# Optimization experiments

Hardware: AMD Instinct MI355X
Metric: run time of the kernel (lower is better)

Reference implementation:

```python
import jax, jax.numpy as jnp
import numpy as np

M, K, N = 2048, 4096, 11008
Q_ABS_MAX = 128.0  # x_scaled_abs_max_fp for w8a8
Q_MIN, Q_MAX = -128, 127


def setup_inputs() -> dict:
    key = jax.random.key(0)
    k1, k2, k3, k4 = jax.random.split(key, 4)
    x = jax.random.normal(k1, (M, K), dtype=jnp.float32)
    # pre-quantized int8 weight, stored [K, N] (transposed layout as in quantize_weights)
    w_q = jax.random.randint(k2, (K, N), Q_MIN, Q_MAX + 1, dtype=jnp.int32).astype(jnp.int8)
    bias = jax.random.normal(k3, (N,), dtype=jnp.float32) * 0.01
    # per-tensor weight dequant scale (q_scale of the quantized weight)
    y_scale = jax.random.uniform(k4, (1,), dtype=jnp.float32, minval=0.001, maxval=0.02)
    return {"x": x, "w_q": w_q, "bias": bias, "y_scale": y_scale}


def reference(x, w_q, bias, y_scale):
    # dynamic per-tensor activation quantization: scale = max|x| / 128
    x_scale = jnp.max(jnp.abs(x)) / jnp.float32(Q_ABS_MAX)
    x_q = jnp.clip(jnp.round(x / x_scale), Q_MIN, Q_MAX).astype(jnp.int8)
    c = jnp.matmul(x_q.astype(jnp.int32), w_q.astype(jnp.int32))
    # dequantize + bias
    y = c.astype(jnp.float32) * (x_scale * y_scale[0]) + bias
    return y
```

## Files before the change

### kernel.cpp

```cpp
#include <hip/hip_runtime.h>
#include <stdint.h>

#define M_DIM 2048
#define K_DIM 4096
#define N_DIM 11008

typedef int v4i __attribute__((ext_vector_type(4)));

#define WS_XQ_OFF   65536ull
#define WS_WT_OFF   8454144ull
#define WS_FULL_BYTES (8454144ull + 45088768ull)
#define WS_SMALL_BYTES 8454144ull

static __device__ __forceinline__ void llds16(const void* g, void* l) {
  __builtin_amdgcn_global_load_lds(
      reinterpret_cast<const uint32_t __attribute__((address_space(1)))*>(
          reinterpret_cast<uintptr_t>(g)),
      reinterpret_cast<uint32_t __attribute__((address_space(3)))*>(
          reinterpret_cast<uintptr_t>(l)),
      16, 0, 0);
}

__global__ __launch_bounds__(256) void absmax_kernel(const float* __restrict__ x,
                                                     float* __restrict__ part) {
  __shared__ float red[256];
  const int g = blockIdx.x * 256 + threadIdx.x;
  const float4* x4 = reinterpret_cast<const float4*>(x);
  float m = 0.f;
#pragma unroll
  for (int i = 0; i < 8; ++i) {
    float4 v = x4[(size_t)i * 262144 + g];
    m = fmaxf(m, fmaxf(fmaxf(fabsf(v.x), fabsf(v.y)),
                       fmaxf(fabsf(v.z), fabsf(v.w))));
  }
  red[threadIdx.x] = m;
  __syncthreads();
  for (int s = 128; s > 0; s >>= 1) {
    if (threadIdx.x < s) red[threadIdx.x] = fmaxf(red[threadIdx.x], red[threadIdx.x + s]);
    __syncthreads();
  }
  if (threadIdx.x == 0) part[blockIdx.x] = red[0];
}

__global__ __launch_bounds__(256) void finalize_scale(const float* __restrict__ part,
                                                      const float* __restrict__ y_scale,
                                                      float* __restrict__ scales) {
  __shared__ float red[256];
  const int t = threadIdx.x;
  float m = fmaxf(fmaxf(part[t], part[t + 256]), fmaxf(part[t + 512], part[t + 768]));
  red[t] = m;
  __syncthreads();
  for (int s = 128; s > 0; s >>= 1) {
    if (t < s) red[t] = fmaxf(red[t], red[t + s]);
    __syncthreads();
  }
  if (t == 0) {
    float xs = red[0] * (1.0f / 128.0f);
    scales[0] = xs;
    scales[1] = xs * y_scale[0];
  }
}

__global__ __launch_bounds__(256) void quant_kernel(const float* __restrict__ x,
                                                    const float* __restrict__ scales,
                                                    signed char* __restrict__ xq) {
  const float s = scales[0];
  const size_t t = (size_t)blockIdx.x * 256 + threadIdx.x;
  const float4* x4 = reinterpret_cast<const float4*>(x) + t * 4;
  v4i o;
#pragma unroll
  for (int i = 0; i < 4; ++i) {
    float4 v = x4[i];
    int q0 = (int)rintf(v.x / s);
    int q1 = (int)rintf(v.y / s);
    int q2 = (int)rintf(v.z / s);
    int q3 = (int)rintf(v.w / s);
    q0 = max(-128, min(127, q0));
    q1 = max(-128, min(127, q1));
    q2 = max(-128, min(127, q2));
    q3 = max(-128, min(127, q3));
    o[i] = (q0 & 255) | ((q1 & 255) << 8) | ((q2 & 255) << 16) | ((q3 & 255) << 24);
  }
  *reinterpret_cast<v4i*>(xq + t * 16) = o;
}

__global__ __launch_bounds__(256) void transpose_pack(const int* __restrict__ w,
                                                      signed char* __restrict__ wt) {
  __shared__ int tile[64 * 65];
  const int t = threadIdx.x;
  const int n0 = blockIdx.x * 64;
  const int k0 = blockIdx.y * 64;
#pragma unroll
  for (int p = 0; p < 4; ++p) {
    const int id = p * 256 + t;
    const int r = id >> 4;
    const int c4 = id & 15;
    v4i v = *reinterpret_cast<const v4i*>(w + (size_t)(k0 + r) * N_DIM + n0 + c4 * 4);
    tile[r * 65 + c4 * 4 + 0] = v[0];
    tile[r * 65 + c4 * 4 + 1] = v[1];
    tile[r * 65 + c4 * 4 + 2] = v[2];
    tile[r * 65 + c4 * 4 + 3] = v[3];
  }
  __syncthreads();
  const int nl = t >> 2;
  const int kseg = t & 3;
  v4i o;
#pragma unroll
  for (int q = 0; q < 4; ++q) {
    const int kb = kseg * 16 + q * 4;
    int b0 = tile[(kb + 0) * 65 + nl] & 255;
    int b1 = tile[(kb + 1) * 65 + nl] & 255;
    int b2 = tile[(kb + 2) * 65 + nl] & 255;
    int b3 = tile[(kb + 3) * 65 + nl] & 255;
    o[q] = b0 | (b1 << 8) | (b2 << 16) | (b3 << 24);
  }
  *reinterpret_cast<v4i*>(wt + (size_t)(n0 + nl) * K_DIM + k0 + kseg * 16) = o;
}

#define V4_TILE_B 24576
#define V4_NT     (K_DIM / 64)

__global__ __launch_bounds__(512, 4) void gemm_i8_v4(
    const signed char* __restrict__ xq, const signed char* __restrict__ wt,
    const float* __restrict__ scales, const float* __restrict__ bias,
    float* __restrict__ y) {
  __shared__ __align__(16) signed char smem[3 * V4_TILE_B];
  const int tid = threadIdx.x;

  const int bid = blockIdx.x;
  const int swz = (bid & 7) * 86 + (bid >> 3);
  const int m0 = (swz & 15) * 128;
  const int n0 = (swz >> 4) * 256;

  const int srow = tid >> 2;
  const int sseg = tid & 3;
  const int sgoff = (sseg ^ ((srow >> 1) & 3)) * 16;
  const signed char* gA  = xq + (size_t)(m0 + srow) * K_DIM + sgoff;
  const signed char* gB0 = wt + (size_t)(n0 + srow) * K_DIM + sgoff;
  const signed char* gB1 = wt + (size_t)(n0 + 128 + srow) * K_DIM + sgoff;
  signed char* const ldA  = smem + tid * 16;
  signed char* const ldB0 = smem + 8192 + tid * 16;
  signed char* const ldB1 = smem + 16384 + tid * 16;

#define STAGE(kt, soff)                                   \
  do {                                                    \
    const size_t ko_ = (size_t)(kt) * 64;                 \
    llds16(gA + ko_,  ldA + (soff));                      \
    llds16(gB0 + ko_, ldB0 + (soff));                     \
    llds16(gB1 + ko_, ldB1 + (soff));                     \
  } while (0)

  const int lane = tid & 63;
  const int wid = tid >> 6;
  const int wm = wid >> 2;
  const int wn = wid & 3;
  const int l15 = lane & 15;
  const int kc = lane >> 4;
  const int segoff = (kc ^ ((l15 >> 1) & 3)) * 16;
  const int offA = (wm * 64 + l15) * 64 + segoff;
  const int offB = 8192 + (wn * 64 + l15) * 64 + segoff;

  v4i acc[4][4] = {};

#define COMPUTE(roff)                                                        \
  do {                                                                       \
    const signed char* bp_ = smem + (roff);                                  \
    v4i a_[4], b_[4];                                                        \
    _Pragma("unroll")                                                        \
    for (int m_ = 0; m_ < 4; ++m_)                                           \
      a_[m_] = *reinterpret_cast<const v4i*>(bp_ + offA + m_ * 1024);        \
    _Pragma("unroll")                                                        \
    for (int n_ = 0; n_ < 4; ++n_)                                           \
      b_[n_] = *reinterpret_cast<const v4i*>(bp_ + offB + n_ * 1024);        \
    _Pragma("unroll")                                                        \
    for (int m_ = 0; m_ < 4; ++m_)                                           \
      _Pragma("unroll")                                                      \
      for (int n_ = 0; n_ < 4; ++n_)                                         \
        acc[m_][n_] = __builtin_amdgcn_mfma_i32_16x16x64_i8(                 \
            a_[m_], b_[n_], acc[m_][n_], 0, 0, 0);                           \
  } while (0)

  STAGE(0, 0);
  STAGE(1, V4_TILE_B);
  asm volatile("s_waitcnt vmcnt(3)" ::: "memory");
  __builtin_amdgcn_s_barrier();

  int rOff = 0;
  int sOff = 2 * V4_TILE_B;
  for (int t = 0; t < V4_NT - 2; ++t) {
    STAGE(t + 2, sOff);
    COMPUTE(rOff);
    asm volatile("s_waitcnt vmcnt(3)" ::: "memory");
    __builtin_amdgcn_s_barrier();
    rOff = (rOff == 2 * V4_TILE_B) ? 0 : rOff + V4_TILE_B;
    sOff = (sOff == 2 * V4_TILE_B) ? 0 : sOff + V4_TILE_B;
  }
  COMPUTE(rOff);
  asm volatile("s_waitcnt vmcnt(0)" ::: "memory");
  __builtin_amdgcn_s_barrier();
  rOff = (rOff == 2 * V4_TILE_B) ? 0 : rOff + V4_TILE_B;
  COMPUTE(rOff);

#undef STAGE
#undef COMPUTE

  const float s = scales[1];
#pragma unroll
  for (int n = 0; n < 4; ++n) {
    const int col = n0 + wn * 64 + n * 16 + l15;
    const float bv = bias[col];
#pragma unroll
    for (int m = 0; m < 4; ++m) {
      const int r0 = m0 + wm * 64 + m * 16 + kc * 4;
#pragma unroll
      for (int j = 0; j < 4; ++j)
        y[(size_t)(r0 + j) * N_DIM + col] = (float)acc[m][n][j] * s + bv;
    }
  }
}

#if defined(__has_builtin)
#if __has_builtin(__builtin_amdgcn_sdot4)
#define HAVE_SDOT4 1
#endif
#endif

static __device__ __forceinline__ int dot4(int a, int b, int c) {
#ifdef HAVE_SDOT4
  return __builtin_amdgcn_sdot4(a, b, c, false);
#else
  c += (int)(signed char)(a) * (int)(signed char)(b);
  c += (int)(signed char)(a >> 8) * (int)(signed char)(b >> 8);
  c += (int)(signed char)(a >> 16) * (int)(signed char)(b >> 16);
  c += (int)(signed char)(a >> 24) * (int)(signed char)(b >> 24);
  return c;
#endif
}

__global__ __launch_bounds__(256) void gemm_fallback(
    const signed char* __restrict__ xq, const int* __restrict__ w,
    const float* __restrict__ scales, const float* __restrict__ bias,
    float* __restrict__ y) {
  __shared__ int lds_a[64 * 17];
  __shared__ int lds_b[64 * 17];
  const int t = threadIdx.x;
  const int m0 = blockIdx.y * 64;
  const int n0 = blockIdx.x * 64;
  const int my = (t >> 4) * 4;
  const int nx = (t & 15) * 4;
  int acc[4][4] = {};
  for (int kt = 0; kt < K_DIM / 64; ++kt) {
    const int k0 = kt * 64;
    {
      const int r = t >> 2, sg = t & 3;
      v4i v = *reinterpret_cast<const v4i*>(xq + (size_t)(m0 + r) * K_DIM + k0 + sg * 16);
      lds_a[r * 17 + sg * 4 + 0] = v[0];
      lds_a[r * 17 + sg * 4 + 1] = v[1];
      lds_a[r * 17 + sg * 4 + 2] = v[2];
      lds_a[r * 17 + sg * 4 + 3] = v[3];
    }
    {
      const int n = t & 63, bkk = (t >> 6) * 4;
#pragma unroll
      for (int q = 0; q < 4; ++q) {
        const int kk = bkk + q;
        int b0 = w[(size_t)(k0 + kk * 4 + 0) * N_DIM + n0 + n] & 255;
        int b1 = w[(size_t)(k0 + kk * 4 + 1) * N_DIM + n0 + n] & 255;
        int b2 = w[(size_t)(k0 + kk * 4 + 2) * N_DIM + n0 + n] & 255;
        int b3 = w[(size_t)(k0 + kk * 4 + 3) * N_DIM + n0 + n] & 255;
        lds_b[n * 17 + kk] = b0 | (b1 << 8) | (b2 << 16) | (b3 << 24);
      }
    }
    __syncthreads();
#pragma unroll
    for (int kk = 0; kk < 16; ++kk) {
      int a[4], b[4];
#pragma unroll
      for (int i = 0; i < 4; ++i) a[i] = lds_a[(my + i) * 17 + kk];
#pragma unroll
      for (int j = 0; j < 4; ++j) b[j] = lds_b[(nx + j) * 17 + kk];
#pragma unroll
      for (int i = 0; i < 4; ++i)
#pragma unroll
        for (int j = 0; j < 4; ++j) acc[i][j] = dot4(a[i], b[j], acc[i][j]);
    }
    __syncthreads();
  }
  const float s = scales[1];
#pragma unroll
  for (int i = 0; i < 4; ++i)
#pragma unroll
    for (int j = 0; j < 4; ++j)
      y[(size_t)(m0 + my + i) * N_DIM + n0 + nx + j] =
          (float)acc[i][j] * s + bias[n0 + nx + j];
}

extern "C" void kernel_launch(void* const* d_in, const int* in_sizes, int n_in,
                              void* d_out, int out_size, void* d_ws, size_t ws_size,
                              hipStream_t stream) {
  (void)in_sizes; (void)n_in; (void)out_size;
  const float* x = (const float*)d_in[0];
  const int* w = (const int*)d_in[1];
  const float* bias = (const float*)d_in[2];
  const float* yscale = (const float*)d_in[3];
  float* y = (float*)d_out;
  char* ws = (char*)d_ws;
  float* scales = (float*)(ws);
  float* part = (float*)(ws + 1024);
  signed char* xq = (signed char*)(ws + WS_XQ_OFF);
  signed char* wt = (signed char*)(ws + WS_WT_OFF);

  if (ws_size < WS_SMALL_BYTES) return;

  absmax_kernel<<<1024, 256, 0, stream>>>(x, part);
  finalize_scale<<<1, 256, 0, stream>>>(part, yscale, scales);
  quant_kernel<<<2048, 256, 0, stream>>>(x, scales, xq);
  if (ws_size >= WS_FULL_BYTES) {
    transpose_pack<<<dim3(N_DIM / 64, K_DIM / 64), 256, 0, stream>>>(w, wt);
    gemm_i8_v4<<<(M_DIM / 128) * (N_DIM / 256), 512, 0, stream>>>(xq, wt, scales, bias, y);
  } else {
    gemm_fallback<<<dim3(N_DIM / 64, M_DIM / 64), 256, 0, stream>>>(xq, w, scales, bias, y);
  }
}
```

Before: 169.3 us.

## Shrink GEMM tile to 128x128 with 4 waves, unroll ring buffer, add setprio

The int8 GEMM block tile drops from 128x256 with 8 waves to 128x128 with 4 waves, doubling the grid, and the block swizzle is adjusted to match. The triple-buffer loop is fully unrolled by three so LDS offsets are constants rather than runtime selects. s_setprio is raised around the MFMA burst so math waves are favoured over loading waves. Smaller tiles give more blocks and better wave occupancy, but they reduce reuse of the A tile and increase global traffic per flop.

```diff
diff --git a/kernel.cpp b/kernel.cpp
--- a/kernel.cpp
+++ b/kernel.cpp
@@ -117,48 +117,47 @@
   *reinterpret_cast<v4i*>(wt + (size_t)(n0 + nl) * K_DIM + k0 + kseg * 16) = o;
 }
 
-#define V4_TILE_B 24576
-#define V4_NT     (K_DIM / 64)
-
-__global__ __launch_bounds__(512, 4) void gemm_i8_v4(
+#define V5_TILE_B 16384
+#define V5_NT     (K_DIM / 64)
+
+__global__ __launch_bounds__(256, 4) void gemm_i8_v5(
     const signed char* __restrict__ xq, const signed char* __restrict__ wt,
     const float* __restrict__ scales, const float* __restrict__ bias,
     float* __restrict__ y) {
-  __shared__ __align__(16) signed char smem[3 * V4_TILE_B];
+  __shared__ __align__(16) signed char smem[3 * V5_TILE_B];
   const int tid = threadIdx.x;
 
   const int bid = blockIdx.x;
-  const int swz = (bid & 7) * 86 + (bid >> 3);
+  const int swz = (bid & 7) * 172 + (bid >> 3);
   const int m0 = (swz & 15) * 128;
-  const int n0 = (swz >> 4) * 256;
+  const int n0 = (swz >> 4) * 128;
 
   const int srow = tid >> 2;
   const int sseg = tid & 3;
   const int sgoff = (sseg ^ ((srow >> 1) & 3)) * 16;
-  const signed char* gA  = xq + (size_t)(m0 + srow) * K_DIM + sgoff;
-  const signed char* gB0 = wt + (size_t)(n0 + srow) * K_DIM + sgoff;
-  const signed char* gB1 = wt + (size_t)(n0 + 128 + srow) * K_DIM + sgoff;
-  signed char* const ldA  = smem + tid * 16;
-  signed char* const ldB0 = smem + 8192 + tid * 16;
-  signed char* const ldB1 = smem + 16384 + tid * 16;
-
-#define STAGE(kt, soff)                                   \
-  do {                                                    \
-    const size_t ko_ = (size_t)(kt) * 64;                 \
-    llds16(gA + ko_,  ldA + (soff));                      \
-    llds16(gB0 + ko_, ldB0 + (soff));                     \
-    llds16(gB1 + ko_, ldB1 + (soff));                     \
+  const signed char* gA = xq + (size_t)(m0 + srow) * K_DIM + sgoff;
+  const signed char* gB = wt + (size_t)(n0 + srow) * K_DIM + sgoff;
+  signed char* const ldA = smem + tid * 16;
+  signed char* const ldB = smem + 8192 + tid * 16;
+
+#define STAGE(kt, soff)                                     \
+  do {                                                      \
+    const size_t ko_ = (size_t)(kt) * 64;                   \
+    llds16(gA + ko_,                      ldA + (soff));    \
+    llds16(gA + ko_ + (size_t)64 * K_DIM, ldA + (soff) + 4096); \
+    llds16(gB + ko_,                      ldB + (soff));    \
+    llds16(gB + ko_ + (size_t)64 * K_DIM, ldB + (soff) + 4096); \
   } while (0)
 
   const int lane = tid & 63;
   const int wid = tid >> 6;
-  const int wm = wid >> 2;
-  const int wn = wid & 3;
+  const int wr = wid >> 1;
+  const int wc = wid & 1;
   const int l15 = lane & 15;
   const int kc = lane >> 4;
   const int segoff = (kc ^ ((l15 >> 1) & 3)) * 16;
-  const int offA = (wm * 64 + l15) * 64 + segoff;
-  const int offB = 8192 + (wn * 64 + l15) * 64 + segoff;
+  const int offA = (wr * 64 + l15) * 64 + segoff;
+  const int offB = 8192 + (wc * 64 + l15) * 64 + segoff;
 
   v4i acc[4][4] = {};
 
@@ -172,46 +171,53 @@
     _Pragma("unroll")                                                        \
     for (int n_ = 0; n_ < 4; ++n_)                                           \
       b_[n_] = *reinterpret_cast<const v4i*>(bp_ + offB + n_ * 1024);        \
+    __builtin_amdgcn_s_setprio(1);                                           \
     _Pragma("unroll")                                                        \
     for (int m_ = 0; m_ < 4; ++m_)                                           \
       _Pragma("unroll")                                                      \
       for (int n_ = 0; n_ < 4; ++n_)                                         \
         acc[m_][n_] = __builtin_amdgcn_mfma_i32_16x16x64_i8(                 \
             a_[m_], b_[n_], acc[m_][n_], 0, 0, 0);                           \
+    __builtin_amdgcn_s_setprio(0);                                           \
   } while (0)
 
+#define ITER(R, S, kt2)                                     \
+  do {                                                      \
+    STAGE((kt2), (S));                                      \
+    COMPUTE((R));                                           \
+    asm volatile("s_waitcnt vmcnt(4)" ::: "memory");        \
+    __builtin_amdgcn_s_barrier();                           \
+  } while (0)
+
   STAGE(0, 0);
-  STAGE(1, V4_TILE_B);
-  asm volatile("s_waitcnt vmcnt(3)" ::: "memory");
+  STAGE(1, V5_TILE_B);
+  asm volatile("s_waitcnt vmcnt(4)" ::: "memory");
   __builtin_amdgcn_s_barrier();
 
-  int rOff = 0;
-  int sOff = 2 * V4_TILE_B;
-  for (int t = 0; t < V4_NT - 2; ++t) {
-    STAGE(t + 2, sOff);
-    COMPUTE(rOff);
-    asm volatile("s_waitcnt vmcnt(3)" ::: "memory");
-    __builtin_amdgcn_s_barrier();
-    rOff = (rOff == 2 * V4_TILE_B) ? 0 : rOff + V4_TILE_B;
-    sOff = (sOff == 2 * V4_TILE_B) ? 0 : sOff + V4_TILE_B;
-  }
-  COMPUTE(rOff);
+  for (int t = 0; t < 60; t += 3) {
+    ITER(0,              2 * V5_TILE_B, t + 2);
+    ITER(V5_TILE_B,      0,             t + 3);
+    ITER(2 * V5_TILE_B,  V5_TILE_B,     t + 4);
+  }
+  ITER(0,         2 * V5_TILE_B, 62);
+  ITER(V5_TILE_B, 0,             63);
+  COMPUTE(2 * V5_TILE_B);
   asm volatile("s_waitcnt vmcnt(0)" ::: "memory");
   __builtin_amdgcn_s_barrier();
-  rOff = (rOff == 2 * V4_TILE_B) ? 0 : rOff + V4_TILE_B;
-  COMPUTE(rOff);
+  COMPUTE(0);
 
 #undef STAGE
 #undef COMPUTE
+#undef ITER
 
   const float s = scales[1];
 #pragma unroll
   for (int n = 0; n < 4; ++n) {
-    const int col = n0 + wn * 64 + n * 16 + l15;
+    const int col = n0 + wc * 64 + n * 16 + l15;
     const float bv = bias[col];
 #pragma unroll
     for (int m = 0; m < 4; ++m) {
-      const int r0 = m0 + wm * 64 + m * 16 + kc * 4;
+      const int r0 = m0 + wr * 64 + m * 16 + kc * 4;
 #pragma unroll
       for (int j = 0; j < 4; ++j)
         y[(size_t)(r0 + j) * N_DIM + col] = (float)acc[m][n][j] * s + bv;
@@ -317,7 +323,7 @@
   quant_kernel<<<2048, 256, 0, stream>>>(x, scales, xq);
   if (ws_size >= WS_FULL_BYTES) {
     transpose_pack<<<dim3(N_DIM / 64, K_DIM / 64), 256, 0, stream>>>(w, wt);
-    gemm_i8_v4<<<(M_DIM / 128) * (N_DIM / 256), 512, 0, stream>>>(xq, wt, scales, bias, y);
+    gemm_i8_v5<<<(M_DIM / 128) * (N_DIM / 128), 256, 0, stream>>>(xq, wt, scales, bias, y);
   } else {
     gemm_fallback<<<dim3(N_DIM / 64, M_DIM / 64), 256, 0, stream>>>(xq, w, scales, bias, y);
   }
```

Measured after the change: 186.6 us. 10.2% more time.

## Pre-pack operands into MFMA fragment order and switch to 32x32x32 int8 MFMA

Applied to the files above, without the earlier changes.

The quantize and weight-transpose kernels now write A and B directly in the per-tile, per-lane fragment order the GEMM consumes. Each stage load becomes one contiguous 16-byte-per-thread copy, and the XOR swizzle is no longer needed. The GEMM switches from 16x16x64 MFMAs with a 4x4 accumulator grid to 32x32x32 MFMAs with a 2x2 grid, which cuts LDS reads per MFMA. In exchange the packing kernels have more complex index math, and the epilogue stores follow the 32x32 output layout.

```diff
diff --git a/kernel.cpp b/kernel.cpp
--- a/kernel.cpp
+++ b/kernel.cpp
@@ -5,7 +5,8 @@
 #define K_DIM 4096
 #define N_DIM 11008
 
-typedef int v4i __attribute__((ext_vector_type(4)));
+typedef int v4i  __attribute__((ext_vector_type(4)));
+typedef int v16i __attribute__((ext_vector_type(16)));
 
 #define WS_XQ_OFF   65536ull
 #define WS_WT_OFF   8454144ull
@@ -61,26 +62,44 @@
   }
 }
 
-__global__ __launch_bounds__(256) void quant_kernel(const float* __restrict__ x,
-                                                    const float* __restrict__ scales,
-                                                    signed char* __restrict__ xq) {
+static __device__ __forceinline__ int quant4(float4 v, float s) {
+  int q0 = (int)rintf(v.x / s);
+  int q1 = (int)rintf(v.y / s);
+  int q2 = (int)rintf(v.z / s);
+  int q3 = (int)rintf(v.w / s);
+  q0 = max(-128, min(127, q0));
+  q1 = max(-128, min(127, q1));
+  q2 = max(-128, min(127, q2));
+  q3 = max(-128, min(127, q3));
+  return (q0 & 255) | ((q1 & 255) << 8) | ((q2 & 255) << 16) | ((q3 & 255) << 24);
+}
+
+__global__ __launch_bounds__(256) void quant_pack(const float* __restrict__ x,
+                                                  const float* __restrict__ scales,
+                                                  signed char* __restrict__ xq) {
+  const float s = scales[0];
+  const int g = blockIdx.x * 256 + threadIdx.x;
+  const int mblk = g >> 15;
+  const int kt = (g >> 9) & 63;
+  const int u = g & 511;
+  const int row = mblk * 128 + ((u >> 7) & 3) * 32 + (u & 31);
+  const int kf = kt * 64 + ((u >> 6) & 1) * 32 + ((u >> 5) & 1) * 16;
+  const float4* xp = reinterpret_cast<const float4*>(x + (size_t)row * K_DIM + kf);
+  v4i o;
+#pragma unroll
+  for (int i = 0; i < 4; ++i) o[i] = quant4(xp[i], s);
+  *reinterpret_cast<v4i*>(xq + (size_t)g * 16) = o;
+}
+
+__global__ __launch_bounds__(256) void quant_rowmajor(const float* __restrict__ x,
+                                                      const float* __restrict__ scales,
+                                                      signed char* __restrict__ xq) {
   const float s = scales[0];
   const size_t t = (size_t)blockIdx.x * 256 + threadIdx.x;
   const float4* x4 = reinterpret_cast<const float4*>(x) + t * 4;
   v4i o;
 #pragma unroll
-  for (int i = 0; i < 4; ++i) {
-    float4 v = x4[i];
-    int q0 = (int)rintf(v.x / s);
-    int q1 = (int)rintf(v.y / s);
-    int q2 = (int)rintf(v.z / s);
-    int q3 = (int)rintf(v.w / s);
-    q0 = max(-128, min(127, q0));
-    q1 = max(-128, min(127, q1));
-    q2 = max(-128, min(127, q2));
-    q3 = max(-128, min(127, q3));
-    o[i] = (q0 & 255) | ((q1 & 255) << 8) | ((q2 & 255) << 16) | ((q3 & 255) << 24);
-  }
+  for (int i = 0; i < 4; ++i) o[i] = quant4(x4[i], s);
   *reinterpret_cast<v4i*>(xq + t * 16) = o;
 }
 
@@ -88,8 +107,10 @@
                                                       signed char* __restrict__ wt) {
   __shared__ int tile[64 * 65];
   const int t = threadIdx.x;
-  const int n0 = blockIdx.x * 64;
-  const int k0 = blockIdx.y * 64;
+  const int bx = blockIdx.x;
+  const int by = blockIdx.y;
+  const int n0 = bx * 64;
+  const int k0 = by * 64;
 #pragma unroll
   for (int p = 0; p < 4; ++p) {
     const int id = p * 256 + t;
@@ -102,119 +123,115 @@
     tile[r * 65 + c4 * 4 + 3] = v[3];
   }
   __syncthreads();
-  const int nl = t >> 2;
-  const int kseg = t & 3;
+  const int nl = ((t >> 7) << 5) | (t & 31);
+  const int kc = (t >> 5) & 3;
   v4i o;
 #pragma unroll
   for (int q = 0; q < 4; ++q) {
-    const int kb = kseg * 16 + q * 4;
+    const int kb = kc * 16 + q * 4;
     int b0 = tile[(kb + 0) * 65 + nl] & 255;
     int b1 = tile[(kb + 1) * 65 + nl] & 255;
     int b2 = tile[(kb + 2) * 65 + nl] & 255;
     int b3 = tile[(kb + 3) * 65 + nl] & 255;
     o[q] = b0 | (b1 << 8) | (b2 << 16) | (b3 << 24);
   }
-  *reinterpret_cast<v4i*>(wt + (size_t)(n0 + nl) * K_DIM + k0 + kseg * 16) = o;
-}
-
-#define V4_TILE_B 24576
-#define V4_NT     (K_DIM / 64)
-
-__global__ __launch_bounds__(512, 4) void gemm_i8_v4(
+  const size_t base = ((size_t)(bx >> 2) * 64 + by) * 16384;
+  const int ubase = ((bx & 3) * 2) << 7;
+  *reinterpret_cast<v4i*>(wt + base + (size_t)(ubase + t) * 16) = o;
+}
+
+#define V8_TILE_B 24576
+#define V8_NT     (K_DIM / 64)
+
+__global__ __launch_bounds__(512, 4) void gemm_i8_v8(
     const signed char* __restrict__ xq, const signed char* __restrict__ wt,
     const float* __restrict__ scales, const float* __restrict__ bias,
     float* __restrict__ y) {
-  __shared__ __align__(16) signed char smem[3 * V4_TILE_B];
+  __shared__ __align__(16) signed char smem[3 * V8_TILE_B];
   const int tid = threadIdx.x;
 
   const int bid = blockIdx.x;
   const int swz = (bid & 7) * 86 + (bid >> 3);
-  const int m0 = (swz & 15) * 128;
-  const int n0 = (swz >> 4) * 256;
-
-  const int srow = tid >> 2;
-  const int sseg = tid & 3;
-  const int sgoff = (sseg ^ ((srow >> 1) & 3)) * 16;
-  const signed char* gA  = xq + (size_t)(m0 + srow) * K_DIM + sgoff;
-  const signed char* gB0 = wt + (size_t)(n0 + srow) * K_DIM + sgoff;
-  const signed char* gB1 = wt + (size_t)(n0 + 128 + srow) * K_DIM + sgoff;
-  signed char* const ldA  = smem + tid * 16;
-  signed char* const ldB0 = smem + 8192 + tid * 16;
-  signed char* const ldB1 = smem + 16384 + tid * 16;
-
-#define STAGE(kt, soff)                                   \
-  do {                                                    \
-    const size_t ko_ = (size_t)(kt) * 64;                 \
-    llds16(gA + ko_,  ldA + (soff));                      \
-    llds16(gB0 + ko_, ldB0 + (soff));                     \
-    llds16(gB1 + ko_, ldB1 + (soff));                     \
+  const int mblk = swz & 15;
+  const int nblk = swz >> 4;
+  const int m0 = mblk * 128;
+  const int n0 = nblk * 256;
+
+  const signed char* gA = xq + (size_t)mblk * 64 * 8192;
+  const signed char* gB = wt + (size_t)nblk * 64 * 16384;
+  signed char* const ld = smem + tid * 16;
+
+#define STAGE(kt, soff)                                                   \
+  do {                                                                    \
+    llds16(gA + (size_t)(kt) * 8192 + tid * 16,         ld + (soff));     \
+    llds16(gB + (size_t)(kt) * 16384 + tid * 16,        ld + (soff) + 8192);  \
+    llds16(gB + (size_t)(kt) * 16384 + 8192 + tid * 16, ld + (soff) + 16384); \
   } while (0)
 
   const int lane = tid & 63;
   const int wid = tid >> 6;
   const int wm = wid >> 2;
   const int wn = wid & 3;
-  const int l15 = lane & 15;
-  const int kc = lane >> 4;
-  const int segoff = (kc ^ ((l15 >> 1) & 3)) * 16;
-  const int offA = (wm * 64 + l15) * 64 + segoff;
-  const int offB = 8192 + (wn * 64 + l15) * 64 + segoff;
-
-  v4i acc[4][4] = {};
-
-#define COMPUTE(roff)                                                        \
-  do {                                                                       \
-    const signed char* bp_ = smem + (roff);                                  \
-    v4i a_[4], b_[4];                                                        \
-    _Pragma("unroll")                                                        \
-    for (int m_ = 0; m_ < 4; ++m_)                                           \
-      a_[m_] = *reinterpret_cast<const v4i*>(bp_ + offA + m_ * 1024);        \
-    _Pragma("unroll")                                                        \
-    for (int n_ = 0; n_ < 4; ++n_)                                           \
-      b_[n_] = *reinterpret_cast<const v4i*>(bp_ + offB + n_ * 1024);        \
-    _Pragma("unroll")                                                        \
-    for (int m_ = 0; m_ < 4; ++m_)                                           \
-      _Pragma("unroll")                                                      \
-      for (int n_ = 0; n_ < 4; ++n_)                                         \
-        acc[m_][n_] = __builtin_amdgcn_mfma_i32_16x16x64_i8(                 \
-            a_[m_], b_[n_], acc[m_][n_], 0, 0, 0);                           \
+  const int aoff = (wm * 2) * 2048 + lane * 16;
+  const int boff = 8192 + (wn * 2) * 2048 + lane * 16;
+
+  v16i acc[2][2] = {};
+
+#define COMPUTE(roff)                                                         \
+  do {                                                                        \
+    const signed char* bp_ = smem + (roff);                                   \
+    _Pragma("unroll")                                                         \
+    for (int ks_ = 0; ks_ < 2; ++ks_) {                                       \
+      v4i a0 = *reinterpret_cast<const v4i*>(bp_ + aoff + ks_ * 1024);        \
+      v4i a1 = *reinterpret_cast<const v4i*>(bp_ + aoff + 2048 + ks_ * 1024); \
+      v4i b0 = *reinterpret_cast<const v4i*>(bp_ + boff + ks_ * 1024);        \
+      v4i b1 = *reinterpret_cast<const v4i*>(bp_ + boff + 2048 + ks_ * 1024); \
+      acc[0][0] = __builtin_amdgcn_mfma_i32_32x32x32_i8(a0, b0, acc[0][0], 0, 0, 0); \
+      acc[0][1] = __builtin_amdgcn_mfma_i32_32x32x32_i8(a0, b1, acc[0][1], 0, 0, 0); \
+      acc[1][0] = __builtin_amdgcn_mfma_i32_32x32x32_i8(a1, b0, acc[1][0], 0, 0, 0); \
+      acc[1][1] = __builtin_amdgcn_mfma_i32_32x32x32_i8(a1, b1, acc[1][1], 0, 0, 0); \
+    }                                                                         \
   } while (0)
 
   STAGE(0, 0);
-  STAGE(1, V4_TILE_B);
+  STAGE(1, V8_TILE_B);
   asm volatile("s_waitcnt vmcnt(3)" ::: "memory");
   __builtin_amdgcn_s_barrier();
 
   int rOff = 0;
-  int sOff = 2 * V4_TILE_B;
-  for (int t = 0; t < V4_NT - 2; ++t) {
+  int sOff = 2 * V8_TILE_B;
+  for (int t = 0; t < V8_NT - 2; ++t) {
     STAGE(t + 2, sOff);
     COMPUTE(rOff);
     asm volatile("s_waitcnt vmcnt(3)" ::: "memory");
     __builtin_amdgcn_s_barrier();
-    rOff = (rOff == 2 * V4_TILE_B) ? 0 : rOff + V4_TILE_B;
-    sOff = (sOff == 2 * V4_TILE_B) ? 0 : sOff + V4_TILE_B;
+    rOff = (rOff == 2 * V8_TILE_B) ? 0 : rOff + V8_TILE_B;
+    sOff = (sOff == 2 * V8_TILE_B) ? 0 : sOff + V8_TILE_B;
   }
   COMPUTE(rOff);
   asm volatile("s_waitcnt vmcnt(0)" ::: "memory");
   __builtin_amdgcn_s_barrier();
-  rOff = (rOff == 2 * V4_TILE_B) ? 0 : rOff + V4_TILE_B;
+  rOff = (rOff == 2 * V8_TILE_B) ? 0 : rOff + V8_TILE_B;
   COMPUTE(rOff);
 
 #undef STAGE
 #undef COMPUTE
 
   const float s = scales[1];
-#pragma unroll
-  for (int n = 0; n < 4; ++n) {
-    const int col = n0 + wn * 64 + n * 16 + l15;
+  const int l31 = lane & 31;
+  const int lh4 = (lane >> 5) * 4;
+#pragma unroll
+  for (int fb = 0; fb < 2; ++fb) {
+    const int col = n0 + wn * 64 + fb * 32 + l31;
     const float bv = bias[col];
 #pragma unroll
-    for (int m = 0; m < 4; ++m) {
-      const int r0 = m0 + wm * 64 + m * 16 + kc * 4;
-#pragma unroll
-      for (int j = 0; j < 4; ++j)
-        y[(size_t)(r0 + j) * N_DIM + col] = (float)acc[m][n][j] * s + bv;
+    for (int fa = 0; fa < 2; ++fa) {
+      const int rbase = m0 + wm * 64 + fa * 32 + lh4;
+#pragma unroll
+      for (int reg = 0; reg < 16; ++reg) {
+        const int row = rbase + (reg & 3) + 8 * (reg >> 2);
+        y[(size_t)row * N_DIM + col] = (float)acc[fa][fb][reg] * s + bv;
+      }
     }
   }
 }
@@ -314,11 +331,12 @@
 
   absmax_kernel<<<1024, 256, 0, stream>>>(x, part);
   finalize_scale<<<1, 256, 0, stream>>>(part, yscale, scales);
-  quant_kernel<<<2048, 256, 0, stream>>>(x, scales, xq);
   if (ws_size >= WS_FULL_BYTES) {
+    quant_pack<<<2048, 256, 0, stream>>>(x, scales, xq);
     transpose_pack<<<dim3(N_DIM / 64, K_DIM / 64), 256, 0, stream>>>(w, wt);
-    gemm_i8_v4<<<(M_DIM / 128) * (N_DIM / 256), 512, 0, stream>>>(xq, wt, scales, bias, y);
+    gemm_i8_v8<<<(M_DIM / 128) * (N_DIM / 256), 512, 0, stream>>>(xq, wt, scales, bias, y);
   } else {
+    quant_rowmajor<<<2048, 256, 0, stream>>>(x, scales, xq);
     gemm_fallback<<<dim3(N_DIM / 64, M_DIM / 64), 256, 0, stream>>>(xq, w, scales, bias, y);
   }
 }
```

Measured after the change: 158.9 us (median of 3 runs). 6.1% less time.
